# Kernel optimization log

Hardware: AMD Instinct MI355X
Metric: run time of the kernel (lower is better)

## Reference

```python
import jax, jax.numpy as jnp
import numpy as np

INPUT_DIM = 512
OUTPUT_DIM = 512
GRID_SIZE = 16
INPUT_MIN = -1.0
INPUT_RANGE = 2.0


def setup_inputs() -> dict:
    key = jax.random.key(0)
    k_x, k_mix = jax.random.split(key)
    x = jax.random.normal(k_x, (65536, INPUT_DIM), dtype=jnp.float32)
    # per-dim spline tables: bases init zeros, slopes init 0.1 (as in torch)
    bases = jnp.zeros((INPUT_DIM, GRID_SIZE), dtype=jnp.float32)
    slopes = jnp.full((INPUT_DIM, GRID_SIZE), 0.1, dtype=jnp.float32)
    mix = jax.random.normal(k_mix, (OUTPUT_DIM, INPUT_DIM), dtype=jnp.float32) * 0.01
    bias = jnp.zeros((OUTPUT_DIM,), dtype=jnp.float32)
    return {"x": x, "bases": bases, "slopes": slopes, "mix": mix, "bias": bias}


def reference(x, bases, slopes, mix, bias):
    # x: [B, D]; bases/slopes: [D, G]; mix: [O, D]; bias: [O]
    B, D = x.shape
    G = bases.shape[1]
    x_norm = jnp.clip((x - INPUT_MIN) / INPUT_RANGE, 0.0, 1.0 - 1e-6)
    idx = jnp.clip((x_norm * G).astype(jnp.int32), 0, G - 1)        # [B, D]
    x_local = x_norm * G - idx.astype(x.dtype)                       # fractional position in cell
    # gather per-dim table entries: flatten [D, G] and index with d*G + idx
    flat_idx = jnp.arange(D, dtype=jnp.int32)[None, :] * G + idx    # [B, D]
    base = bases.reshape(-1)[flat_idx]                               # [B, D]
    slope = slopes.reshape(-1)[flat_idx]                             # [B, D]
    spline_out = base + slope * x_local                              # [B, D]
    y = jnp.einsum('bd,od->bo', spline_out, mix) + bias              # [B, O]
    return y
```

## Files before the change

kernel.cpp:

```cpp
#include <hip/hip_runtime.h>


#define DIMK 512
#define DIMN 512
#define GRID_G 16

typedef unsigned short u16;
typedef unsigned int u32;
typedef __attribute__((ext_vector_type(8))) __bf16 bf16x8;
typedef __attribute__((ext_vector_type(4))) float f32x4;

__device__ __forceinline__ u32 bf16rne(float f) {
    u32 u = __float_as_uint(f);
    return (u + 0x7fffu + ((u >> 16) & 1u)) >> 16;
}

__global__ void prep_kernel(const float* __restrict__ mix,
                            u16* __restrict__ mixb) {
    int t = blockIdx.x * 256 + threadIdx.x;
    float4 v = reinterpret_cast<const float4*>(mix)[t];
    ushort4 o;
    o.x = (u16)bf16rne(v.x);
    o.y = (u16)bf16rne(v.y);
    o.z = (u16)bf16rne(v.z);
    o.w = (u16)bf16rne(v.w);
    reinterpret_cast<ushort4*>(mixb)[t] = o;
}

__global__ __launch_bounds__(512, 2) void kan_kernel(
    const float* __restrict__ x, const float* __restrict__ bases,
    const float* __restrict__ slopes, const u16* __restrict__ mixb,
    const float* __restrict__ bias, float* __restrict__ y) {
    __shared__ u32 s_tab[DIMK * 17];
    __shared__ __align__(16) u16 sA[128 * 32];
    __shared__ __align__(16) u16 sB[512 * 32];

    const int tid = threadIdx.x;
    const int lane = tid & 63;
    const int wid = tid >> 6;
    const int quad = lane >> 4;
    const int l15 = lane & 15;
    const int wave_m = wid >> 2;
    const int wave_n = wid & 3;
    const int m0 = blockIdx.x * 128;

#pragma unroll
    for (int k = 0; k < 16; k++) {
        int i = tid + k * 512;
        u32 p = bf16rne(bases[i]) | (bf16rne(slopes[i]) << 16);
        s_tab[(i >> 4) * 17 + (i & 15)] = p;
    }

    const int ar = tid >> 2;
    const int akg = tid & 3;
    const int awchunk = (ar << 2) | (akg ^ ((ar >> 1) & 3));
    const float4* xrow =
        reinterpret_cast<const float4*>(x + (size_t)(m0 + ar) * DIMK) + akg * 2;

    f32x4 acc[4][8];
#pragma unroll
    for (int i = 0; i < 4; i++)
#pragma unroll
        for (int j = 0; j < 8; j++) acc[i][j] = (f32x4){0.f, 0.f, 0.f, 0.f};

    float4 xa = xrow[0];
    float4 xb = xrow[1];

    __syncthreads();

    for (int kt = 0; kt < 16; ++kt) {
        float xs[8] = {xa.x, xa.y, xa.z, xa.w, xb.x, xb.y, xb.z, xb.w};
        const int dbase = kt * 32 + akg * 8;
        u32 h[8];
#pragma unroll
        for (int j = 0; j < 8; j++) {
            float xn = fminf(fmaxf((xs[j] + 1.0f) * 0.5f, 0.0f), 0.999999f);
            float tt = xn * 16.0f;
            int idx = (int)tt;
            u32 p = s_tab[(dbase + j) * 17 + idx];
            float base = __uint_as_float(p << 16);
            float slope = __uint_as_float(p & 0xffff0000u);
            float sp = fmaf(slope, tt - (float)idx, base);
            h[j] = bf16rne(sp);
        }
        int4 pk = make_int4((int)(h[0] | (h[1] << 16)), (int)(h[2] | (h[3] << 16)),
                            (int)(h[4] | (h[5] << 16)), (int)(h[6] | (h[7] << 16)));
        *reinterpret_cast<int4*>(&sA[awchunk * 8]) = pk;

#pragma unroll
        for (int i = 0; i < 4; i++) {
            int grp = wid * 4 + i;
            int n = grp * 16 + (lane >> 2);
            int c = (lane & 3) ^ ((n >> 1) & 3);
            const u16* gsrc = mixb + (size_t)n * DIMK + kt * 32 + c * 8;
            __builtin_amdgcn_global_load_lds(
                (const __attribute__((address_space(1))) void*)gsrc,
                (__attribute__((address_space(3))) void*)(&sB[grp * 512]),
                16, 0, 0);
        }
        __syncthreads();

        if (kt < 15) {
            xa = xrow[(kt + 1) * 8];
            xb = xrow[(kt + 1) * 8 + 1];
        }

        bf16x8 afrag[4];
#pragma unroll
        for (int fm = 0; fm < 4; fm++) {
            int m_l = wave_m * 64 + fm * 16 + l15;
            int ci = (m_l << 2) | (quad ^ ((m_l >> 1) & 3));
            afrag[fm] = *reinterpret_cast<const bf16x8*>(&sA[ci * 8]);
        }
#pragma unroll
        for (int fn = 0; fn < 8; fn++) {
            int n_l = wave_n * 128 + fn * 16 + l15;
            int ci = (n_l << 2) | (quad ^ ((n_l >> 1) & 3));
            bf16x8 bfrag = *reinterpret_cast<const bf16x8*>(&sB[ci * 8]);
#pragma unroll
            for (int fm = 0; fm < 4; fm++)
                acc[fm][fn] = __builtin_amdgcn_mfma_f32_16x16x32_bf16(
                    afrag[fm], bfrag, acc[fm][fn], 0, 0, 0);
        }
        __syncthreads();
    }

#pragma unroll
    for (int fn = 0; fn < 8; fn++) {
        int o = wave_n * 128 + fn * 16 + l15;
        float bv = bias[o];
#pragma unroll
        for (int fm = 0; fm < 4; fm++) {
            int row = m0 + wave_m * 64 + fm * 16 + quad * 4;
            float* yp = y + (size_t)row * DIMN + o;
#pragma unroll
            for (int j = 0; j < 4; j++)
                yp[(size_t)j * DIMN] = acc[fm][fn][j] + bv;
        }
    }
}

extern "C" void kernel_launch(void* const* d_in, const int* in_sizes, int n_in,
                              void* d_out, int out_size, void* d_ws, size_t ws_size,
                              hipStream_t stream) {
    const float* x = (const float*)d_in[0];
    const float* bases = (const float*)d_in[1];
    const float* slopes = (const float*)d_in[2];
    const float* mix = (const float*)d_in[3];
    const float* bias = (const float*)d_in[4];
    float* y = (float*)d_out;

    u16* mixb = (u16*)d_ws;

    hipLaunchKernelGGL(prep_kernel, dim3(256), dim3(256), 0, stream, mix, mixb);
    hipLaunchKernelGGL(kan_kernel, dim3(512), dim3(512), 0, stream,
                       x, bases, slopes, mixb, bias, y);
}
```

Measured before the change: 262.7 us.

## Pre-swizzle mix into MFMA fragment layout and drop LDS staging for GEMM operands

```diff
diff --git a/kernel.cpp b/kernel.cpp
--- a/kernel.cpp
+++ b/kernel.cpp
@@ -3,7 +3,6 @@
 
 #define DIMK 512
 #define DIMN 512
-#define GRID_G 16
 
 typedef unsigned short u16;
 typedef unsigned int u32;
@@ -18,13 +17,41 @@
 __global__ void prep_kernel(const float* __restrict__ mix,
                             u16* __restrict__ mixb) {
     int t = blockIdx.x * 256 + threadIdx.x;
-    float4 v = reinterpret_cast<const float4*>(mix)[t];
-    ushort4 o;
-    o.x = (u16)bf16rne(v.x);
-    o.y = (u16)bf16rne(v.y);
-    o.z = (u16)bf16rne(v.z);
-    o.w = (u16)bf16rne(v.w);
-    reinterpret_cast<ushort4*>(mixb)[t] = o;
+    int lane = t & 63;
+    int gk = t >> 6;
+    int kt = gk & 15;
+    int g = gk >> 4;
+    int n = g * 16 + (lane & 15);
+    int d = kt * 32 + (lane >> 4) * 8;
+    const float4* src = reinterpret_cast<const float4*>(mix + (size_t)n * DIMK + d);
+    float4 a = src[0];
+    float4 b = src[1];
+    ushort4 lo, hi;
+    lo.x = (u16)bf16rne(a.x); lo.y = (u16)bf16rne(a.y);
+    lo.z = (u16)bf16rne(a.z); lo.w = (u16)bf16rne(a.w);
+    hi.x = (u16)bf16rne(b.x); hi.y = (u16)bf16rne(b.y);
+    hi.z = (u16)bf16rne(b.z); hi.w = (u16)bf16rne(b.w);
+    ushort4* dst = reinterpret_cast<ushort4*>(mixb + (size_t)t * 8);
+    dst[0] = lo;
+    dst[1] = hi;
+}
+
+__device__ __forceinline__ bf16x8 spline8(float4 a, float4 b,
+                                          const u32* tab, int dbase) {
+    float xs[8] = {a.x, a.y, a.z, a.w, b.x, b.y, b.z, b.w};
+    bf16x8 r;
+#pragma unroll
+    for (int j = 0; j < 8; j++) {
+        float xn = fminf(fmaxf((xs[j] + 1.0f) * 0.5f, 0.0f), 0.999999f);
+        float tt = xn * 16.0f;
+        int idx = (int)tt;
+        u32 p = tab[(dbase + j) * 17 + idx];
+        float base = __uint_as_float(p << 16);
+        float slope = __uint_as_float(p & 0xffff0000u);
+        float sp = fmaf(slope, tt - (float)idx, base);
+        r[j] = (__bf16)sp;
+    }
+    return r;
 }
 
 __global__ __launch_bounds__(512, 2) void kan_kernel(
@@ -32,16 +59,14 @@
     const float* __restrict__ slopes, const u16* __restrict__ mixb,
     const float* __restrict__ bias, float* __restrict__ y) {
     __shared__ u32 s_tab[DIMK * 17];
-    __shared__ __align__(16) u16 sA[128 * 32];
-    __shared__ __align__(16) u16 sB[512 * 32];
 
     const int tid = threadIdx.x;
     const int lane = tid & 63;
     const int wid = tid >> 6;
     const int quad = lane >> 4;
     const int l15 = lane & 15;
-    const int wave_m = wid >> 2;
-    const int wave_n = wid & 3;
+    const int wave_m = wid >> 1;
+    const int wave_n = wid & 1;
     const int m0 = blockIdx.x * 128;
 
 #pragma unroll
@@ -51,87 +76,69 @@
         s_tab[(i >> 4) * 17 + (i & 15)] = p;
     }
 
-    const int ar = tid >> 2;
-    const int akg = tid & 3;
-    const int awchunk = (ar << 2) | (akg ^ ((ar >> 1) & 3));
-    const float4* xrow =
-        reinterpret_cast<const float4*>(x + (size_t)(m0 + ar) * DIMK) + akg * 2;
+    const float4* xp0 = reinterpret_cast<const float4*>(
+                            x + (size_t)(m0 + wave_m * 32 + l15) * DIMK) +
+                        quad * 2;
+    const float4* xp1 = xp0 + 16 * (DIMK / 4);
 
-    f32x4 acc[4][8];
+    const bf16x8* bp = reinterpret_cast<const bf16x8*>(mixb) +
+                       (size_t)wave_n * 16384 + lane;
+
+    f32x4 acc[2][16];
 #pragma unroll
-    for (int i = 0; i < 4; i++)
+    for (int i = 0; i < 2; i++)
 #pragma unroll
-        for (int j = 0; j < 8; j++) acc[i][j] = (f32x4){0.f, 0.f, 0.f, 0.f};
+        for (int j = 0; j < 16; j++) acc[i][j] = (f32x4){0.f, 0.f, 0.f, 0.f};
 
-    float4 xa = xrow[0];
-    float4 xb = xrow[1];
+    float4 xa0 = xp0[0], xa1 = xp0[1];
+    float4 xb0 = xp1[0], xb1 = xp1[1];
 
     __syncthreads();
 
     for (int kt = 0; kt < 16; ++kt) {
-        float xs[8] = {xa.x, xa.y, xa.z, xa.w, xb.x, xb.y, xb.z, xb.w};
-        const int dbase = kt * 32 + akg * 8;
-        u32 h[8];
+        const int kto = kt * 64;
+
+        const int ktn = ((kt + 1) & 15) * 8;
+        float4 n0 = xp0[ktn], n1 = xp0[ktn + 1];
+        float4 n2 = xp1[ktn], n3 = xp1[ktn + 1];
+
+        bf16x8 bf[8];
 #pragma unroll
-        for (int j = 0; j < 8; j++) {
-            float xn = fminf(fmaxf((xs[j] + 1.0f) * 0.5f, 0.0f), 0.999999f);
-            float tt = xn * 16.0f;
-            int idx = (int)tt;
-            u32 p = s_tab[(dbase + j) * 17 + idx];
-            float base = __uint_as_float(p << 16);
-            float slope = __uint_as_float(p & 0xffff0000u);
-            float sp = fmaf(slope, tt - (float)idx, base);
-            h[j] = bf16rne(sp);
-        }
-        int4 pk = make_int4((int)(h[0] | (h[1] << 16)), (int)(h[2] | (h[3] << 16)),
-                            (int)(h[4] | (h[5] << 16)), (int)(h[6] | (h[7] << 16)));
-        *reinterpret_cast<int4*>(&sA[awchunk * 8]) = pk;
+        for (int fn = 0; fn < 8; fn++) bf[fn] = bp[fn * 1024 + kto];
+
+        const int dbase = kt * 32 + quad * 8;
+        bf16x8 af0 = spline8(xa0, xa1, s_tab, dbase);
+        bf16x8 af1 = spline8(xb0, xb1, s_tab, dbase);
+
+        bf16x8 bg[8];
+#pragma unroll
+        for (int fn = 0; fn < 8; fn++) bg[fn] = bp[(8 + fn) * 1024 + kto];
 
 #pragma unroll
-        for (int i = 0; i < 4; i++) {
-            int grp = wid * 4 + i;
-            int n = grp * 16 + (lane >> 2);
-            int c = (lane & 3) ^ ((n >> 1) & 3);
-            const u16* gsrc = mixb + (size_t)n * DIMK + kt * 32 + c * 8;
-            __builtin_amdgcn_global_load_lds(
-                (const __attribute__((address_space(1))) void*)gsrc,
-                (__attribute__((address_space(3))) void*)(&sB[grp * 512]),
-                16, 0, 0);
-        }
-        __syncthreads();
-
-        if (kt < 15) {
-            xa = xrow[(kt + 1) * 8];
-            xb = xrow[(kt + 1) * 8 + 1];
-        }
-
-        bf16x8 afrag[4];
-#pragma unroll
-        for (int fm = 0; fm < 4; fm++) {
-            int m_l = wave_m * 64 + fm * 16 + l15;
-            int ci = (m_l << 2) | (quad ^ ((m_l >> 1) & 3));
-            afrag[fm] = *reinterpret_cast<const bf16x8*>(&sA[ci * 8]);
+        for (int fn = 0; fn < 8; fn++) {
+            acc[0][fn] = __builtin_amdgcn_mfma_f32_16x16x32_bf16(
+                af0, bf[fn], acc[0][fn], 0, 0, 0);
+            acc[1][fn] = __builtin_amdgcn_mfma_f32_16x16x32_bf16(
+                af1, bf[fn], acc[1][fn], 0, 0, 0);
         }
 #pragma unroll
         for (int fn = 0; fn < 8; fn++) {
-            int n_l = wave_n * 128 + fn * 16 + l15;
-            int ci = (n_l << 2) | (quad ^ ((n_l >> 1) & 3));
-            bf16x8 bfrag = *reinterpret_cast<const bf16x8*>(&sB[ci * 8]);
-#pragma unroll
-            for (int fm = 0; fm < 4; fm++)
-                acc[fm][fn] = __builtin_amdgcn_mfma_f32_16x16x32_bf16(
-                    afrag[fm], bfrag, acc[fm][fn], 0, 0, 0);
+            acc[0][8 + fn] = __builtin_amdgcn_mfma_f32_16x16x32_bf16(
+                af0, bg[fn], acc[0][8 + fn], 0, 0, 0);
+            acc[1][8 + fn] = __builtin_amdgcn_mfma_f32_16x16x32_bf16(
+                af1, bg[fn], acc[1][8 + fn], 0, 0, 0);
         }
-        __syncthreads();
+
+        xa0 = n0; xa1 = n1; xb0 = n2; xb1 = n3;
     }
 
 #pragma unroll
-    for (int fn = 0; fn < 8; fn++) {
-        int o = wave_n * 128 + fn * 16 + l15;
+    for (int fn = 0; fn < 16; fn++) {
+        int o = wave_n * 256 + fn * 16 + l15;
         float bv = bias[o];
 #pragma unroll
-        for (int fm = 0; fm < 4; fm++) {
-            int row = m0 + wave_m * 64 + fm * 16 + quad * 4;
+        for (int fm = 0; fm < 2; fm++) {
+            int row = m0 + wave_m * 32 + fm * 16 + quad * 4;
             float* yp = y + (size_t)row * DIMN + o;
 #pragma unroll
             for (int j = 0; j < 4; j++)
@@ -152,7 +159,7 @@
 
     u16* mixb = (u16*)d_ws;
 
-    hipLaunchKernelGGL(prep_kernel, dim3(256), dim3(256), 0, stream, mix, mixb);
+    hipLaunchKernelGGL(prep_kernel, dim3(128), dim3(256), 0, stream, mix, mixb);
     hipLaunchKernelGGL(kan_kernel, dim3(512), dim3(512), 0, stream,
                        x, bases, slopes, mixb, bias, y);
 }
```

Result: slower. 359.6 us (+36.9%).

## Double-buffer spline A tile and mix B tile to overlap staging with MFMA

Applied to the files above, without the earlier changes.

```diff
diff --git a/kernel.cpp b/kernel.cpp
--- a/kernel.cpp
+++ b/kernel.cpp
@@ -3,7 +3,6 @@
 
 #define DIMK 512
 #define DIMN 512
-#define GRID_G 16
 
 typedef unsigned short u16;
 typedef unsigned int u32;
@@ -32,8 +31,8 @@
     const float* __restrict__ slopes, const u16* __restrict__ mixb,
     const float* __restrict__ bias, float* __restrict__ y) {
     __shared__ u32 s_tab[DIMK * 17];
-    __shared__ __align__(16) u16 sA[128 * 32];
-    __shared__ __align__(16) u16 sB[512 * 32];
+    __shared__ __align__(16) u16 sA[2][128 * 32];
+    __shared__ __align__(16) u16 sB[2][512 * 32];
 
     const int tid = threadIdx.x;
     const int lane = tid & 63;
@@ -63,13 +62,8 @@
 #pragma unroll
         for (int j = 0; j < 8; j++) acc[i][j] = (f32x4){0.f, 0.f, 0.f, 0.f};
 
-    float4 xa = xrow[0];
-    float4 xb = xrow[1];
-
-    __syncthreads();
-
-    for (int kt = 0; kt < 16; ++kt) {
-        float xs[8] = {xa.x, xa.y, xa.z, xa.w, xb.x, xb.y, xb.z, xb.w};
+    auto stage_a = [&](u16* sAb, float4 a, float4 b, int kt) {
+        float xs[8] = {a.x, a.y, a.z, a.w, b.x, b.y, b.z, b.w};
         const int dbase = kt * 32 + akg * 8;
         u32 h[8];
 #pragma unroll
@@ -85,8 +79,9 @@
         }
         int4 pk = make_int4((int)(h[0] | (h[1] << 16)), (int)(h[2] | (h[3] << 16)),
                             (int)(h[4] | (h[5] << 16)), (int)(h[6] | (h[7] << 16)));
-        *reinterpret_cast<int4*>(&sA[awchunk * 8]) = pk;
-
+        *reinterpret_cast<int4*>(&sAb[awchunk * 8]) = pk;
+    };
+    auto stage_b = [&](u16* sBb, int kt) {
 #pragma unroll
         for (int i = 0; i < 4; i++) {
             int grp = wid * 4 + i;
@@ -95,34 +90,54 @@
             const u16* gsrc = mixb + (size_t)n * DIMK + kt * 32 + c * 8;
             __builtin_amdgcn_global_load_lds(
                 (const __attribute__((address_space(1))) void*)gsrc,
-                (__attribute__((address_space(3))) void*)(&sB[grp * 512]),
+                (__attribute__((address_space(3))) void*)(&sBb[grp * 512]),
                 16, 0, 0);
         }
-        __syncthreads();
+    };
+
+    float4 p0 = xrow[0], p1 = xrow[1];
+    __syncthreads();
+    stage_a(&sA[0][0], p0, p1, 0);
+    stage_b(&sB[0][0], 0);
+    float4 xs0a = xrow[8], xs0b = xrow[9];
+    __syncthreads();
+
+    int cur = 0;
+    for (int kt = 0; kt < 16; ++kt) {
+        float4 xna = xs0a, xnb = xs0b;
+        if (kt < 14) {
+            xna = xrow[(kt + 2) * 8];
+            xnb = xrow[(kt + 2) * 8 + 1];
+        }
 
         if (kt < 15) {
-            xa = xrow[(kt + 1) * 8];
-            xb = xrow[(kt + 1) * 8 + 1];
+            stage_a(&sA[cur ^ 1][0], xs0a, xs0b, kt + 1);
+            stage_b(&sB[cur ^ 1][0], kt + 1);
         }
 
+        const u16* sAc = &sA[cur][0];
+        const u16* sBc = &sB[cur][0];
         bf16x8 afrag[4];
 #pragma unroll
         for (int fm = 0; fm < 4; fm++) {
             int m_l = wave_m * 64 + fm * 16 + l15;
             int ci = (m_l << 2) | (quad ^ ((m_l >> 1) & 3));
-            afrag[fm] = *reinterpret_cast<const bf16x8*>(&sA[ci * 8]);
+            afrag[fm] = *reinterpret_cast<const bf16x8*>(&sAc[ci * 8]);
         }
 #pragma unroll
         for (int fn = 0; fn < 8; fn++) {
             int n_l = wave_n * 128 + fn * 16 + l15;
             int ci = (n_l << 2) | (quad ^ ((n_l >> 1) & 3));
-            bf16x8 bfrag = *reinterpret_cast<const bf16x8*>(&sB[ci * 8]);
+            bf16x8 bfrag = *reinterpret_cast<const bf16x8*>(&sBc[ci * 8]);
 #pragma unroll
             for (int fm = 0; fm < 4; fm++)
                 acc[fm][fn] = __builtin_amdgcn_mfma_f32_16x16x32_bf16(
                     afrag[fm], bfrag, acc[fm][fn], 0, 0, 0);
         }
-        __syncthreads();
+
+        if (kt < 15) __syncthreads();
+        xs0a = xna; xs0b = xnb;
+        cur ^= 1;
     }
 
 #pragma unroll
```

New measurement: 260.8 us. No clear change (-0.7%).
